# Kernel optimization log

Measured on AMD Instinct MI355X. Metric: run time of the kernel, lower is better.

The kernel has to match this reference:

```python
import jax, jax.numpy as jnp
import numpy as np

N = 8192
D = 512


def setup_inputs() -> dict:
    key = jax.random.key(0)
    k1, k2, k3, k4 = jax.random.split(key, 4)
    U = jax.random.normal(k1, (N, D), dtype=jnp.float32)
    V = jax.random.normal(k2, (N, D), dtype=jnp.float32)
    M = jax.random.normal(k3, (N, N), dtype=jnp.float32)
    W = jax.random.uniform(k4, (N, N), dtype=jnp.float32)
    alpha = jnp.ones((1,), dtype=jnp.float32) * 0.1
    return {"U": U, "V": V, "M": M, "W": W, "alpha": alpha}


def reference(U, V, M, W, alpha):
    # Reconstruction term: sum((U V^T - M)^2)
    recon = U @ V.T                                  # (N, N) GEMM
    part1 = jnp.sum(jnp.square(recon - M))
    # Manifold term in closed form:
    # sum_{i,j} W[i,j] * ||U_i - V_j||^2
    #   = sum_i rowW_i ||U_i||^2 + sum_j colW_j ||V_j||^2 - 2 sum(W * U V^T)
    u_sq = jnp.sum(U * U, axis=1)                    # (N,)
    v_sq = jnp.sum(V * V, axis=1)                    # (N,)
    row_w = jnp.sum(W, axis=1)                       # (N,)
    col_w = jnp.sum(W, axis=0)                       # (N,)
    cross = jnp.sum(W * recon)
    part2 = alpha[0] * (jnp.dot(row_w, u_sq) + jnp.dot(col_w, v_sq) - 2.0 * cross)
    total = part1 + part2
    return total / (M.shape[0] * M.shape[1])
```

## Files before the change

### kernel.cpp

```cpp
#include <hip/hip_runtime.h>
#include <hip/hip_bf16.h>
#include <stdint.h>

#define N_DIM 8192
#define D_DIM 512
#define BM 128
#define BN 128
#define BK 64
#define RSTR 140
#define TPB 4

typedef __attribute__((ext_vector_type(8))) short bf16x8;
typedef __attribute__((ext_vector_type(4))) float f32x4;
typedef __attribute__((ext_vector_type(4))) unsigned int u32x4;

__device__ __forceinline__ unsigned short f2bf(float f) {
    unsigned int x = __float_as_uint(f);
    x += 0x7fffu + ((x >> 16) & 1u);
    return (unsigned short)(x >> 16);
}
__device__ __forceinline__ float bf2f(unsigned short u) {
    return __uint_as_float(((unsigned int)u) << 16);
}

__global__ void __launch_bounds__(256) prep_kernel(
    const float* __restrict__ U, const float* __restrict__ V,
    unsigned short* __restrict__ Ub, unsigned short* __restrict__ Vb,
    float* __restrict__ usq, float* __restrict__ vsq)
{
    int row = blockIdx.x;
    const float* src;
    unsigned short* dst;
    float* sq;
    if (row < N_DIM) {
        src = U + (size_t)row * D_DIM;
        dst = Ub + (size_t)row * D_DIM;
        sq  = usq + row;
    } else {
        int r = row - N_DIM;
        src = V + (size_t)r * D_DIM;
        dst = Vb + (size_t)r * D_DIM;
        sq  = vsq + r;
    }
    int t = threadIdx.x;
    float2 v = *reinterpret_cast<const float2*>(src + 2 * t);
    float s = v.x * v.x + v.y * v.y;
    ushort2 b;
    b.x = f2bf(v.x);
    b.y = f2bf(v.y);
    *reinterpret_cast<ushort2*>(dst + 2 * t) = b;

    #pragma unroll
    for (int o = 32; o > 0; o >>= 1) s += __shfl_down(s, o, 64);
    __shared__ float red[4];
    if ((t & 63) == 0) red[t >> 6] = s;
    __syncthreads();
    if (t == 0) *sq = red[0] + red[1] + red[2] + red[3];
}

__global__ void __launch_bounds__(256, 2) fused_kernel(
    const unsigned short* __restrict__ Ub, const unsigned short* __restrict__ Vb,
    const float* __restrict__ Mg, const float* __restrict__ Wg,
    const float* __restrict__ usq, const float* __restrict__ vsq,
    double* __restrict__ acc)
{
    __shared__ alignas(16) char smem[BM * BK * 2 + BN * BK * 2];
    __shared__ alignas(16) unsigned short recs[BM * RSTR];
    __shared__ float red1[4], red2[4];
    char* As = smem;
    char* Bs = smem + BM * BK * 2;

    const int t    = threadIdx.x;
    const int lane = t & 63;
    const int wave = t >> 6;
    const int wm   = wave >> 1;
    const int wn   = wave & 1;

    const int bid    = blockIdx.x;
    const int tile_m = bid >> 4;
    const int quad   = bid & 15;
    const int row0   = tile_m * BM;

    const int rg = t >> 4;
    const int c8 = (t & 15) * 8;

    float s1 = 0.f, s2 = 0.f;

    int   colp = 0;
    f32x4 vs0, vs1;
    f32x4 mA0, mA1, wA0, wA1; float usA;
    f32x4 mB0, mB1, wB0, wB1; float usB;

    auto issueA = [&](int chunk) {
        int r = chunk * 16 + rg;
        const float* Mp = Mg + (size_t)(row0 + r) * N_DIM + colp + c8;
        const float* Wp = Wg + (size_t)(row0 + r) * N_DIM + colp + c8;
        mA0 = *reinterpret_cast<const f32x4*>(Mp);
        mA1 = *reinterpret_cast<const f32x4*>(Mp + 4);
        wA0 = *reinterpret_cast<const f32x4*>(Wp);
        wA1 = *reinterpret_cast<const f32x4*>(Wp + 4);
        usA = usq[row0 + r];
    };
    auto issueB = [&](int chunk) {
        int r = chunk * 16 + rg;
        const float* Mp = Mg + (size_t)(row0 + r) * N_DIM + colp + c8;
        const float* Wp = Wg + (size_t)(row0 + r) * N_DIM + colp + c8;
        mB0 = *reinterpret_cast<const f32x4*>(Mp);
        mB1 = *reinterpret_cast<const f32x4*>(Mp + 4);
        wB0 = *reinterpret_cast<const f32x4*>(Wp);
        wB1 = *reinterpret_cast<const f32x4*>(Wp + 4);
        usB = usq[row0 + r];
    };
    auto consumeA = [&](int chunk) {
        int r = chunk * 16 + rg;
        bf16x8 rb = *reinterpret_cast<const bf16x8*>(&recs[r * RSTR + c8]);
        #pragma unroll
        for (int c = 0; c < 4; ++c) {
            float rc = bf2f((unsigned short)rb[c]);
            float d  = rc - mA0[c];
            s1 = fmaf(d, d, s1);
            s2 = fmaf(wA0[c], usA + vs0[c] - 2.f * rc, s2);
        }
        #pragma unroll
        for (int c = 0; c < 4; ++c) {
            float rc = bf2f((unsigned short)rb[4 + c]);
            float d  = rc - mA1[c];
            s1 = fmaf(d, d, s1);
            s2 = fmaf(wA1[c], usA + vs1[c] - 2.f * rc, s2);
        }
    };
    auto consumeB = [&](int chunk) {
        int r = chunk * 16 + rg;
        bf16x8 rb = *reinterpret_cast<const bf16x8*>(&recs[r * RSTR + c8]);
        #pragma unroll
        for (int c = 0; c < 4; ++c) {
            float rc = bf2f((unsigned short)rb[c]);
            float d  = rc - mB0[c];
            s1 = fmaf(d, d, s1);
            s2 = fmaf(wB0[c], usB + vs0[c] - 2.f * rc, s2);
        }
        #pragma unroll
        for (int c = 0; c < 4; ++c) {
            float rc = bf2f((unsigned short)rb[4 + c]);
            float d  = rc - mB1[c];
            s1 = fmaf(d, d, s1);
            s2 = fmaf(wB1[c], usB + vs1[c] - 2.f * rc, s2);
        }
    };

    auto stage_load = [&](const unsigned short* Ua, const unsigned short* Va, int k0,
                          u32x4 (&sa)[4], u32x4 (&sb)[4]) {
        #pragma unroll
        for (int c = 0; c < 4; ++c) {
            int s   = c * 256 + t;
            int row = s >> 3;
            int kg  = s & 7;
            sa[c] = *reinterpret_cast<const u32x4*>(Ua + (size_t)row * D_DIM + k0 + kg * 8);
            sb[c] = *reinterpret_cast<const u32x4*>(Va + (size_t)row * D_DIM + k0 + kg * 8);
        }
    };
    auto stage_write = [&](u32x4 (&sa)[4], u32x4 (&sb)[4]) {
        #pragma unroll
        for (int c = 0; c < 4; ++c) {
            int s   = c * 256 + t;
            int row = s >> 3;
            int kg  = s & 7;
            int kgs = kg ^ (row & 7);
            *reinterpret_cast<u32x4*>(As + row * (BK * 2) + kgs * 16) = sa[c];
            *reinterpret_cast<u32x4*>(Bs + row * (BK * 2) + kgs * 16) = sb[c];
        }
    };

    auto mma = [&](f32x4 (&a)[4][4]) {
        #pragma unroll
        for (int kc = 0; kc < 2; ++kc) {
            bf16x8 af[4], bfr[4];
            const int kgw = kc * 4 + (lane >> 4);
            #pragma unroll
            for (int i = 0; i < 4; ++i) {
                int ra = wm * 64 + i * 16 + (lane & 15);
                af[i]  = *reinterpret_cast<const bf16x8*>(As + ra * (BK * 2) + ((kgw ^ (ra & 7)) * 16));
                int rb = wn * 64 + i * 16 + (lane & 15);
                bfr[i] = *reinterpret_cast<const bf16x8*>(Bs + rb * (BK * 2) + ((kgw ^ (rb & 7)) * 16));
            }
            #pragma unroll
            for (int i = 0; i < 4; ++i)
                #pragma unroll
                for (int j = 0; j < 4; ++j)
                    a[i][j] = __builtin_amdgcn_mfma_f32_16x16x32_bf16(af[i], bfr[j], a[i][j], 0, 0, 0);
        }
    };

    auto dump = [&](f32x4 (&a)[4][4]) {
        #pragma unroll
        for (int i = 0; i < 4; ++i)
            #pragma unroll
            for (int j = 0; j < 4; ++j)
                #pragma unroll
                for (int q = 0; q < 4; ++q) {
                    int r = wm * 64 + i * 16 + (lane >> 4) * 4 + q;
                    int c = wn * 64 + j * 16 + (lane & 15);
                    recs[r * RSTR + c] = f2bf(a[i][j][q]);
                }
    };

    const f32x4 zero = {0.f, 0.f, 0.f, 0.f};
    const unsigned short* Ua = Ub + (size_t)row0 * D_DIM;
    f32x4 a[4][4];
    u32x4 sa[4], sb[4];

    #define FENCE() asm volatile("" ::: "memory")
    #define LGKM0_BAR() do { \
        asm volatile("s_waitcnt lgkmcnt(0)" ::: "memory"); \
        __builtin_amdgcn_s_barrier(); } while (0)

    for (int it = 0; it < TPB; ++it) {
        const int col0 = (quad * TPB + it) * BN;
        const unsigned short* Va = Vb + (size_t)col0 * D_DIM;
        const bool strm = (it > 0);

        #pragma unroll
        for (int i = 0; i < 4; ++i)
            #pragma unroll
            for (int j = 0; j < 4; ++j) a[i][j] = zero;

        if (strm) {
            colp = col0 - BN;
            vs0 = *reinterpret_cast<const f32x4*>(vsq + colp + c8);
            vs1 = *reinterpret_cast<const f32x4*>(vsq + colp + c8 + 4);
            issueA(0);
        }

        for (int kt2 = 0; kt2 < 4; ++kt2) {
            const int kt = kt2 * 2;
            stage_load(Ua, Va, kt * BK, sa, sb);
            FENCE();
            if (strm) issueB(kt + 1);
            FENCE();
            stage_write(sa, sb);
            LGKM0_BAR();
            mma(a);
            if (strm) consumeA(kt);
            LGKM0_BAR();

            stage_load(Ua, Va, (kt + 1) * BK, sa, sb);
            FENCE();
            if (strm && kt2 < 3) issueA(kt + 2);
            FENCE();
            stage_write(sa, sb);
            LGKM0_BAR();
            mma(a);
            if (strm) consumeB(kt + 1);
            LGKM0_BAR();
        }
        dump(a);
    }

    colp = (quad * TPB + TPB - 1) * BN;
    vs0 = *reinterpret_cast<const f32x4*>(vsq + colp + c8);
    vs1 = *reinterpret_cast<const f32x4*>(vsq + colp + c8 + 4);
    LGKM0_BAR();
    issueA(0);
    issueB(1);
    consumeA(0); issueA(2);
    consumeB(1); issueB(3);
    consumeA(2); issueA(4);
    consumeB(3); issueB(5);
    consumeA(4); issueA(6);
    consumeB(5); issueB(7);
    consumeA(6);
    consumeB(7);

    #pragma unroll
    for (int o = 32; o > 0; o >>= 1) {
        s1 += __shfl_down(s1, o, 64);
        s2 += __shfl_down(s2, o, 64);
    }
    if (lane == 0) { red1[wave] = s1; red2[wave] = s2; }
    __syncthreads();
    if (t == 0) {
        double a1s = (double)red1[0] + red1[1] + red1[2] + red1[3];
        double a2s = (double)red2[0] + red2[1] + red2[2] + red2[3];
        atomicAdd(acc, a1s);
        atomicAdd(acc + 1, a2s);
    }
    #undef FENCE
    #undef LGKM0_BAR
}

__global__ void finalize_kernel(const double* __restrict__ acc,
                                const float* __restrict__ alpha,
                                float* __restrict__ out)
{
    double tot = acc[0] + (double)alpha[0] * acc[1];
    out[0] = (float)(tot / ((double)N_DIM * (double)N_DIM));
}

extern "C" void kernel_launch(void* const* d_in, const int* in_sizes, int n_in,
                              void* d_out, int out_size, void* d_ws, size_t ws_size,
                              hipStream_t stream) {
    const float* U     = (const float*)d_in[0];
    const float* V     = (const float*)d_in[1];
    const float* Mg    = (const float*)d_in[2];
    const float* Wg    = (const float*)d_in[3];
    const float* alpha = (const float*)d_in[4];

    char* ws = (char*)d_ws;
    unsigned short* Ub = (unsigned short*)ws;
    unsigned short* Vb = (unsigned short*)(ws + 8u * 1024 * 1024);
    float* usq = (float*)(ws + 16u * 1024 * 1024);
    float* vsq = (float*)(ws + 16u * 1024 * 1024 + 32u * 1024);
    double* acc = (double*)(ws + 16u * 1024 * 1024 + 64u * 1024);

    hipMemsetAsync(acc, 0, 2 * sizeof(double), stream);
    prep_kernel<<<2 * N_DIM, 256, 0, stream>>>(U, V, Ub, Vb, usq, vsq);
    fused_kernel<<<(N_DIM / BM) * (N_DIM / BN) / TPB, 256, 0, stream>>>(
        Ub, Vb, Mg, Wg, usq, vsq, acc);
    finalize_kernel<<<1, 1, 0, stream>>>(acc, alpha, (float*)d_out);
}
```

Before: 178.7 us.

## Split fused kernel into GEMM waves and dedicated M/W streaming consumer waves

Doubles the block to 512 threads: waves 0-3 do only the bf16 MFMA GEMM and dump the tile to LDS, while waves 4-7 stream M and W for the previous tile and run the loss reduction with a 4-deep register prefetch ring. This warp specialization is meant to overlap the memory-bound M/W streaming with MFMA work without interleaving both in the same waves. In exchange there are more threads per block, launch bounds of 512x4 that may force register pressure or spills, and barriers now shared across both roles.

```diff
diff --git a/kernel.cpp b/kernel.cpp
--- a/kernel.cpp
+++ b/kernel.cpp
@@ -58,7 +58,7 @@
     if (t == 0) *sq = red[0] + red[1] + red[2] + red[3];
 }
 
-__global__ void __launch_bounds__(256, 2) fused_kernel(
+__global__ void __launch_bounds__(512, 4) fused_kernel(
     const unsigned short* __restrict__ Ub, const unsigned short* __restrict__ Vb,
     const float* __restrict__ Mg, const float* __restrict__ Wg,
     const float* __restrict__ usq, const float* __restrict__ vsq,
@@ -66,13 +66,14 @@
 {
     __shared__ alignas(16) char smem[BM * BK * 2 + BN * BK * 2];
     __shared__ alignas(16) unsigned short recs[BM * RSTR];
-    __shared__ float red1[4], red2[4];
+    __shared__ float red1[8], red2[8];
     char* As = smem;
     char* Bs = smem + BM * BK * 2;
 
     const int t    = threadIdx.x;
     const int lane = t & 63;
     const int wave = t >> 6;
+    const bool gw  = (wave < 4);
     const int wm   = wave >> 1;
     const int wn   = wave & 1;
 
@@ -81,70 +82,43 @@
     const int quad   = bid & 15;
     const int row0   = tile_m * BM;
 
-    const int rg = t >> 4;
-    const int c8 = (t & 15) * 8;
+    const int ts = t - 256;
+    const int rg = ts >> 4;
+    const int c8 = (ts & 15) * 8;
 
     float s1 = 0.f, s2 = 0.f;
 
     int   colp = 0;
     f32x4 vs0, vs1;
-    f32x4 mA0, mA1, wA0, wA1; float usA;
-    f32x4 mB0, mB1, wB0, wB1; float usB;
-
-    auto issueA = [&](int chunk) {
+    f32x4 ms0[4], ms1[4], ws0[4], ws1[4];
+    float uss[4];
+
+    auto issue = [&](int chunk, int set) {
         int r = chunk * 16 + rg;
         const float* Mp = Mg + (size_t)(row0 + r) * N_DIM + colp + c8;
         const float* Wp = Wg + (size_t)(row0 + r) * N_DIM + colp + c8;
-        mA0 = *reinterpret_cast<const f32x4*>(Mp);
-        mA1 = *reinterpret_cast<const f32x4*>(Mp + 4);
-        wA0 = *reinterpret_cast<const f32x4*>(Wp);
-        wA1 = *reinterpret_cast<const f32x4*>(Wp + 4);
-        usA = usq[row0 + r];
-    };
-    auto issueB = [&](int chunk) {
-        int r = chunk * 16 + rg;
-        const float* Mp = Mg + (size_t)(row0 + r) * N_DIM + colp + c8;
-        const float* Wp = Wg + (size_t)(row0 + r) * N_DIM + colp + c8;
-        mB0 = *reinterpret_cast<const f32x4*>(Mp);
-        mB1 = *reinterpret_cast<const f32x4*>(Mp + 4);
-        wB0 = *reinterpret_cast<const f32x4*>(Wp);
-        wB1 = *reinterpret_cast<const f32x4*>(Wp + 4);
-        usB = usq[row0 + r];
-    };
-    auto consumeA = [&](int chunk) {
+        ms0[set] = *reinterpret_cast<const f32x4*>(Mp);
+        ms1[set] = *reinterpret_cast<const f32x4*>(Mp + 4);
+        ws0[set] = *reinterpret_cast<const f32x4*>(Wp);
+        ws1[set] = *reinterpret_cast<const f32x4*>(Wp + 4);
+        uss[set] = usq[row0 + r];
+    };
+    auto consume = [&](int chunk, int set) {
         int r = chunk * 16 + rg;
         bf16x8 rb = *reinterpret_cast<const bf16x8*>(&recs[r * RSTR + c8]);
         #pragma unroll
         for (int c = 0; c < 4; ++c) {
             float rc = bf2f((unsigned short)rb[c]);
-            float d  = rc - mA0[c];
+            float d  = rc - ms0[set][c];
             s1 = fmaf(d, d, s1);
-            s2 = fmaf(wA0[c], usA + vs0[c] - 2.f * rc, s2);
+            s2 = fmaf(ws0[set][c], uss[set] + vs0[c] - 2.f * rc, s2);
         }
         #pragma unroll
         for (int c = 0; c < 4; ++c) {
             float rc = bf2f((unsigned short)rb[4 + c]);
-            float d  = rc - mA1[c];
+            float d  = rc - ms1[set][c];
             s1 = fmaf(d, d, s1);
-            s2 = fmaf(wA1[c], usA + vs1[c] - 2.f * rc, s2);
-        }
-    };
-    auto consumeB = [&](int chunk) {
-        int r = chunk * 16 + rg;
-        bf16x8 rb = *reinterpret_cast<const bf16x8*>(&recs[r * RSTR + c8]);
-        #pragma unroll
-        for (int c = 0; c < 4; ++c) {
-            float rc = bf2f((unsigned short)rb[c]);
-            float d  = rc - mB0[c];
-            s1 = fmaf(d, d, s1);
-            s2 = fmaf(wB0[c], usB + vs0[c] - 2.f * rc, s2);
-        }
-        #pragma unroll
-        for (int c = 0; c < 4; ++c) {
-            float rc = bf2f((unsigned short)rb[4 + c]);
-            float d  = rc - mB1[c];
-            s1 = fmaf(d, d, s1);
-            s2 = fmaf(wB1[c], usB + vs1[c] - 2.f * rc, s2);
+            s2 = fmaf(ws1[set][c], uss[set] + vs1[c] - 2.f * rc, s2);
         }
     };
 
@@ -204,72 +178,71 @@
                 }
     };
 
+    #define LGKM0_BAR() do { \
+        asm volatile("s_waitcnt lgkmcnt(0)" ::: "memory"); \
+        __builtin_amdgcn_s_barrier(); } while (0)
+
     const f32x4 zero = {0.f, 0.f, 0.f, 0.f};
     const unsigned short* Ua = Ub + (size_t)row0 * D_DIM;
     f32x4 a[4][4];
     u32x4 sa[4], sb[4];
 
-    #define FENCE() asm volatile("" ::: "memory")
-    #define LGKM0_BAR() do { \
-        asm volatile("s_waitcnt lgkmcnt(0)" ::: "memory"); \
-        __builtin_amdgcn_s_barrier(); } while (0)
-
     for (int it = 0; it < TPB; ++it) {
         const int col0 = (quad * TPB + it) * BN;
         const unsigned short* Va = Vb + (size_t)col0 * D_DIM;
         const bool strm = (it > 0);
 
-        #pragma unroll
-        for (int i = 0; i < 4; ++i)
-            #pragma unroll
-            for (int j = 0; j < 4; ++j) a[i][j] = zero;
-
-        if (strm) {
+        if (gw) {
+            #pragma unroll
+            for (int i = 0; i < 4; ++i)
+                #pragma unroll
+                for (int j = 0; j < 4; ++j) a[i][j] = zero;
+        } else if (strm) {
             colp = col0 - BN;
             vs0 = *reinterpret_cast<const f32x4*>(vsq + colp + c8);
             vs1 = *reinterpret_cast<const f32x4*>(vsq + colp + c8 + 4);
-            issueA(0);
-        }
-
-        for (int kt2 = 0; kt2 < 4; ++kt2) {
-            const int kt = kt2 * 2;
-            stage_load(Ua, Va, kt * BK, sa, sb);
-            FENCE();
-            if (strm) issueB(kt + 1);
-            FENCE();
-            stage_write(sa, sb);
+        }
+
+        #pragma unroll
+        for (int kt = 0; kt < 8; ++kt) {
+            if (gw) {
+                stage_load(Ua, Va, kt * BK, sa, sb);
+                stage_write(sa, sb);
+            } else if (strm) {
+                issue(kt, kt & 3);
+            }
             LGKM0_BAR();
-            mma(a);
-            if (strm) consumeA(kt);
+            if (gw) {
+                mma(a);
+            } else if (strm && kt >= 3) {
+                consume(kt - 3, (kt - 3) & 3);
+            }
             LGKM0_BAR();
-
-            stage_load(Ua, Va, (kt + 1) * BK, sa, sb);
-            FENCE();
-            if (strm && kt2 < 3) issueA(kt + 2);
-            FENCE();
-            stage_write(sa, sb);
-            LGKM0_BAR();
-            mma(a);
-            if (strm) consumeB(kt + 1);
-            LGKM0_BAR();
-        }
-        dump(a);
-    }
-
-    colp = (quad * TPB + TPB - 1) * BN;
-    vs0 = *reinterpret_cast<const f32x4*>(vsq + colp + c8);
-    vs1 = *reinterpret_cast<const f32x4*>(vsq + colp + c8 + 4);
+        }
+        if (!gw && strm) {
+            consume(5, 1);
+            consume(6, 2);
+            consume(7, 3);
+        }
+        LGKM0_BAR();
+        if (gw) dump(a);
+    }
+
     LGKM0_BAR();
-    issueA(0);
-    issueB(1);
-    consumeA(0); issueA(2);
-    consumeB(1); issueB(3);
-    consumeA(2); issueA(4);
-    consumeB(3); issueB(5);
-    consumeA(4); issueA(6);
-    consumeB(5); issueB(7);
-    consumeA(6);
-    consumeB(7);
+    if (!gw) {
+        colp = (quad * TPB + TPB - 1) * BN;
+        vs0 = *reinterpret_cast<const f32x4*>(vsq + colp + c8);
+        vs1 = *reinterpret_cast<const f32x4*>(vsq + colp + c8 + 4);
+        issue(0, 0); issue(1, 1); issue(2, 2);
+        consume(0, 0); issue(3, 3);
+        consume(1, 1); issue(4, 0);
+        consume(2, 2); issue(5, 1);
+        consume(3, 3); issue(6, 2);
+        consume(4, 0); issue(7, 3);
+        consume(5, 1);
+        consume(6, 2);
+        consume(7, 3);
+    }
 
     #pragma unroll
     for (int o = 32; o > 0; o >>= 1) {
@@ -279,12 +252,12 @@
     if (lane == 0) { red1[wave] = s1; red2[wave] = s2; }
     __syncthreads();
     if (t == 0) {
-        double a1s = (double)red1[0] + red1[1] + red1[2] + red1[3];
-        double a2s = (double)red2[0] + red2[1] + red2[2] + red2[3];
+        double a1s = 0.0, a2s = 0.0;
+        #pragma unroll
+        for (int wv = 0; wv < 8; ++wv) { a1s += red1[wv]; a2s += red2[wv]; }
         atomicAdd(acc, a1s);
         atomicAdd(acc + 1, a2s);
     }
-    #undef FENCE
     #undef LGKM0_BAR
 }
 
@@ -314,7 +287,7 @@
 
     hipMemsetAsync(acc, 0, 2 * sizeof(double), stream);
     prep_kernel<<<2 * N_DIM, 256, 0, stream>>>(U, V, Ub, Vb, usq, vsq);
-    fused_kernel<<<(N_DIM / BM) * (N_DIM / BN) / TPB, 256, 0, stream>>>(
+    fused_kernel<<<(N_DIM / BM) * (N_DIM / BN) / TPB, 512, 0, stream>>>(
         Ub, Vb, Mg, Wg, usq, vsq, acc);
     finalize_kernel<<<1, 1, 0, stream>>>(acc, alpha, (float*)d_out);
 }
```

Result: slower. 606.8 us (+239.5%).
